# Optimization experiments

Measured on AMD Instinct MI355X. Metric: run time of the kernel, lower is better.

Reference implementation:

```python
import jax, jax.numpy as jnp
import numpy as np

IOU_THR = 0.5
SCORE_THR = 0.5
MAX_OUT = 300  # max_output_boxes_per_batch


def setup_inputs() -> dict:
    key = jax.random.key(0)
    kb, ks = jax.random.split(key)
    B, N, C = 8, 1024, 32
    u = jax.random.uniform(kb, (B, N, 4), dtype=jnp.float32)
    ctr = u[..., :2] * 100.0          # box centers in [0,100)
    sz = u[..., 2:] * 20.0 + 1.0      # box sizes in [1,21)
    # y1x1y2x2 format (as the torch module expects)
    boxes = jnp.concatenate([ctr - 0.5 * sz, ctr + 0.5 * sz], axis=-1)
    scores = jax.random.uniform(ks, (B, N, C), dtype=jnp.float32)
    return {"boxes": boxes, "scores": scores}


def _pairwise_iou(b):
    # b: [C, N, 4] in y1x1y2x2; IoU is invariant to the axis swap so no
    # conversion to x1y1x2y2 is needed.
    y1, x1, y2, x2 = b[..., 0], b[..., 1], b[..., 2], b[..., 3]
    area = (y2 - y1) * (x2 - x1)                          # [C, N]
    yy1 = jnp.maximum(y1[..., :, None], y1[..., None, :])
    xx1 = jnp.maximum(x1[..., :, None], x1[..., None, :])
    yy2 = jnp.minimum(y2[..., :, None], y2[..., None, :])
    xx2 = jnp.minimum(x2[..., :, None], x2[..., None, :])
    inter = jnp.clip(yy2 - yy1, 0.0) * jnp.clip(xx2 - xx1, 0.0)
    return inter / (area[..., :, None] + area[..., None, :] - inter)


def _nms_keep(iou, valid, thr):
    # Sequential greedy suppression, vectorized across classes.
    # iou: [C, N, N] (score-descending order), valid: [C, N] bool.
    N = iou.shape[-1]
    idx = jnp.arange(N)

    def body(i, keep):
        sup = (iou[:, i, :] > thr) & keep[:, i][:, None] & (idx[None, :] > i)
        return keep & ~sup

    return jax.lax.fori_loop(0, N, body, valid)


def _nms_single(boxes, scores):
    # boxes: [N, 4], scores: [N, C]  ->  ([M,4], [M], [M])
    N, C = scores.shape
    M = MAX_OUT
    sc = scores.T                                  # [C, N]
    valid = sc > SCORE_THR
    s = jnp.where(valid, sc, -jnp.inf)
    order = jnp.argsort(-s, axis=1, stable=True)   # per-class score desc
    sb = boxes[order]                              # [C, N, 4]
    ss = jnp.take_along_axis(s, order, axis=1)     # [C, N]
    sv = jnp.take_along_axis(valid, order, axis=1)
    keep = _nms_keep(_pairwise_iou(sb), sv, IOU_THR)   # [C, N]

    # flatten class-major (matches torch scores.transpose(1,0).flatten())
    fb = sb.reshape(C * N, 4)
    fs = ss.reshape(-1)
    fk = keep.reshape(-1)
    fcls = jnp.repeat(jnp.arange(C, dtype=jnp.int32), N)
    fbind = order.reshape(-1)                      # original box index

    # global score-descending order over kept detections, truncate to M
    g = jnp.where(fk, fs, -jnp.inf)
    gord = jnp.argsort(-g, stable=True)[:M]
    tb, ts, tc, ti, tv = fb[gord], fs[gord], fcls[gord], fbind[gord], fk[gord]

    # dedup by original box index: keep highest-score (first) occurrence;
    # torch's _get_unique_first_indices re-orders by ascending box index.
    p = jnp.arange(M, dtype=jnp.int32)
    first = jnp.full((N,), M, dtype=jnp.int32).at[ti].min(jnp.where(tv, p, M))
    present = first < M                            # [N]
    ordN = jnp.argsort(~present, stable=True)[:M]  # present box ids, ascending
    pos = first[ordN]
    m = present[ordN]
    posc = jnp.where(m, pos, 0)
    out_boxes = jnp.where(m[:, None], tb[posc], 0.0)
    out_scores = jnp.where(m, ts[posc], 0.0)
    out_classes = jnp.where(m, tc[posc], 0)
    return out_boxes, out_scores, out_classes


def reference(boxes, scores):
    ob, osc, ocl = jax.vmap(_nms_single)(boxes, scores)
    # matches torch return (output_boxes, output_scores, output_classes)
    return ob, osc, ocl
```

## Files before the change

### kernel.cpp

```cpp
#include <hip/hip_runtime.h>

#pragma clang fp contract(off)

#define NBOX   1024
#define NCLS   32
#define NBATCH 8
#define MAXOUT 300
#define SMAX   11
#define MAGIC  0x600DF00Du

#define IOU_SUP(ab, aa, bj, arj, act, acc) do {               \
    float yy1 = fmaxf((ab).x, (bj).x);                        \
    float xx1 = fmaxf((ab).y, (bj).y);                        \
    float yy2 = fminf((ab).z, (bj).z);                        \
    float xx2 = fminf((ab).w, (bj).w);                        \
    float ih = fmaxf(yy2 - yy1, 0.0f);                        \
    float iw = fmaxf(xx2 - xx1, 0.0f);                        \
    float inter = ih * iw;                                    \
    float denom = ((aa) + (arj)) - inter;                     \
    float lhs = (inter + inter) - denom;                      \
    float rhs = denom * 5.9604644775390625e-08f;              \
    if ((act) && (lhs > rhs)) (acc) |= bit;                   \
  } while (0)

__device__ __forceinline__ unsigned long long shflx64(unsigned long long v, int m) {
  unsigned lo = (unsigned)__shfl_xor((int)(unsigned)v, m, 64);
  unsigned hi = (unsigned)__shfl_xor((int)(unsigned)(v >> 32), m, 64);
  return ((unsigned long long)hi << 32) | lo;
}

__device__ __forceinline__ unsigned long long cexch(
    unsigned long long mine, int jj, int kk, int t) {
  unsigned long long other = shflx64(mine, jj);
  bool iLow = ((t & jj) == 0);
  bool desc = ((t & kk) == 0);
  bool wantMax = (iLow == desc);
  bool otherBigger = (other > mine);
  return (wantMax == otherBigger) ? other : mine;
}

__global__ __launch_bounds__(1024) void nms_fused(
    const float* __restrict__ boxes, const float* __restrict__ scores,
    unsigned long long* __restrict__ recs, unsigned int* __restrict__ flags,
    float* __restrict__ out) {
#pragma clang fp contract(off)
  const int bc = blockIdx.x;
  const int b = bc & (NBATCH - 1);
  const int c = bc >> 3;
  const int t = threadIdx.x;
  const int lane = t & 63, wav = t >> 6;

  __shared__ __align__(16) unsigned char shraw[63488];
  unsigned long long* key  = (unsigned long long*)shraw;
  float4* sbox             = (float4*)(shraw + 8192);
  float* sarea             = (float*)(shraw + 24576);
  unsigned long long* mask = (unsigned long long*)(shraw + 28672);
  __shared__ unsigned long long kb[16];
  __shared__ int shV;

  const float* sp = scores + (size_t)b * NBOX * NCLS + c;
  float s = sp[(size_t)t * NCLS];
  bool valid = (s > 0.5f);
  unsigned long long mine = valid
      ? ((((unsigned long long)__float_as_uint(s)) << 32) | (unsigned)(NBOX - 1 - t))
      : (unsigned long long)(unsigned)(NBOX - 1 - t);
  if (t == 0) shV = 0;
  if (t < 16) kb[t] = 0ull;
  __syncthreads();
  unsigned long long vb = __ballot(valid);
  if (lane == 0) atomicAdd(&shV, (int)__popcll(vb));

  for (int kk = 2; kk <= 64; kk <<= 1)
    for (int jj = kk >> 1; jj > 0; jj >>= 1)
      mine = cexch(mine, jj, kk, t);
  key[t] = mine;
  __syncthreads();
  for (int kk = 128; kk <= 1024; kk <<= 1) {
    for (int jj = kk >> 1; jj >= 64; jj >>= 1) {
      if (t < 512) {
        int i = ((t & ~(jj - 1)) << 1) | (t & (jj - 1));
        int ixj = i | jj;
        unsigned long long a = key[i], bb = key[ixj];
        if (((i & kk) == 0) ? (a < bb) : (a > bb)) { key[i] = bb; key[ixj] = a; }
      }
      __syncthreads();
    }
    mine = key[t];
    for (int jj = 32; jj > 0; jj >>= 1) mine = cexch(mine, jj, kk, t);
    key[t] = mine;
    __syncthreads();
  }

  int n0 = NBOX - 1 - (int)(mine & (NBOX - 1));
  const float4* gb = (const float4*)boxes + (size_t)b * NBOX;
  float4 bx4 = gb[n0];
  sbox[t] = bx4;
  sarea[t] = (bx4.z - bx4.x) * (bx4.w - bx4.y);
  __syncthreads();
  const int V = shV;
  const int S = (V + 63) >> 6;
  const bool aj = (t < V);

  unsigned long long mext[15];
  unsigned long long mself = 0ull;
#pragma unroll
  for (int w = 0; w < 15; ++w) mext[w] = 0ull;

  if (S <= SMAX) {
    int NC = 0;
    for (int I2 = 0; I2 < S; ++I2) NC += (S - I2 + 2) / 3;
    for (int k = wav; k < NC; k += 16) {
      int I = 0, rem = k;
      for (;;) { int cI = (S - I + 2) / 3; if (rem < cI) break; rem -= cI; ++I; }
      const int J0 = I + 3 * rem;
      const bool h1 = (J0 + 1 < S), h2 = (J0 + 2 < S);
      const int j0 = (J0 << 6) + lane;
      const int j1 = h1 ? j0 + 64 : j0;
      const int j2 = h2 ? j0 + 128 : j0;
      const float4 b0 = sbox[j0]; const float ar0 = sarea[j0];
      const float4 b1 = sbox[j1]; const float ar1 = sarea[j1];
      const float4 b2 = sbox[j2]; const float ar2 = sarea[j2];
      const bool act0 = (j0 < V);
      const bool act1 = h1 && (j0 + 64 < V);
      const bool act2 = h2 && (j0 + 128 < V);
      const float4* bi = &sbox[I << 6];
      const float* ai = &sarea[I << 6];
      unsigned long long a0 = 0, a1 = 0, a2 = 0;
      unsigned long long bit = 1ull;
#pragma unroll 8
      for (int q = 0; q < 64; ++q) {
        float4 ab = bi[q];
        float aa = ai[q];
        IOU_SUP(ab, aa, b0, ar0, act0, a0);
        IOU_SUP(ab, aa, b1, ar1, act1, a1);
        IOU_SUP(ab, aa, b2, ar2, act2, a2);
        bit <<= 1;
      }
      if (rem == 0) a0 &= (1ull << lane) - 1ull;
      const int vrem = V - (I << 6);
      if (vrem < 64) {
        unsigned long long tm = (1ull << vrem) - 1ull;
        a0 &= tm; a1 &= tm; a2 &= tm;
      }
      mask[(((J0 * (J0 + 1) / 2) << 6) + lane * (J0 + 1)) + I] = a0;
      if (h1) mask[((((J0 + 1) * (J0 + 2) / 2) << 6) + lane * (J0 + 2)) + I] = a1;
      if (h2) mask[((((J0 + 2) * (J0 + 3) / 2) << 6) + lane * (J0 + 3)) + I] = a2;
    }
    __syncthreads();
    if (t < (S << 6)) {
      const int J = wav;
      const int rbs = ((J * (J + 1) / 2) << 6) + lane * (J + 1);
#pragma unroll
      for (int I = 0; I < 15; ++I)
        if (I < J) mext[I] = mask[rbs + I];
      mself = mask[rbs + J];
    }
  } else {
    const int J = wav;
    const float4 bj = sbox[t];
    const float arj = sarea[t];
#pragma unroll
    for (int I = 0; I < 16; ++I) {
      if (I <= J && (I << 6) < V) {
        unsigned long long acc = 0, bit = 1ull;
        for (int q = 0; q < 64; ++q) {
          int i = (I << 6) + q;
          float4 ab = sbox[i];
          float aa = sarea[i];
          bool act = aj && (i < t) && (i < V);
          IOU_SUP(ab, aa, bj, arj, act, acc);
          bit <<= 1;
        }
        if (I == J) mself = acc;
        else mext[I] = acc;
      }
    }
  }
  __syncthreads();

  for (int w = 0; w < S; ++w) {
    if (wav == w) {
      bool supExt = false;
#pragma unroll
      for (int i = 0; i < 15; ++i)
        if (i < w) supExt = supExt || ((mext[i] & kb[i]) != 0ull);
      bool alive = aj && !supExt;
      unsigned long long cur = __ballot(alive);
      for (;;) {
        unsigned long long nb = __ballot(alive && ((mself & cur) == 0ull));
        if (nb == cur) break;
        cur = nb;
      }
      if (lane == 0) kb[w] = cur;
    }
    __syncthreads();
  }

  unsigned long long kbr[16];
#pragma unroll
  for (int w = 0; w < 16; ++w) kbr[w] = kb[w];
  int tot = 0;
#pragma unroll
  for (int w = 0; w < 16; ++w) tot += (int)__popcll(kbr[w]);
  const size_t rbase = ((size_t)b * NCLS + c) * MAXOUT;
  unsigned long long kw = kbr[0];
#pragma unroll
  for (int w = 1; w < 16; ++w) if (w == wav) kw = kbr[w];
  if (aj && ((kw >> lane) & 1ull)) {
    int rank = 0;
#pragma unroll
    for (int w = 0; w < 16; ++w)
      if (w < wav) rank += (int)__popcll(kbr[w]);
    rank += (int)__popcll(kw & ((1ull << lane) - 1ull));
    if (rank < MAXOUT) {
      unsigned sbits = (unsigned)(mine >> 32);
      int n = NBOX - 1 - (int)(mine & (NBOX - 1));
      int flat = c * NBOX + t;
      recs[rbase + rank] = (((unsigned long long)sbits) << 32)
          | ((unsigned)(NCLS * NBOX - 1 - flat) << 10) | (unsigned)n;
    }
  }
  if (t < MAXOUT && t >= ((tot < MAXOUT) ? tot : MAXOUT)) recs[rbase + t] = 0ull;

  __syncthreads();
  if (t == 0)
    __hip_atomic_store(&flags[bc], MAGIC, __ATOMIC_RELEASE,
                       __HIP_MEMORY_SCOPE_AGENT);
  if (c != 0) return;

  if (t < NCLS)
    while (__hip_atomic_load(&flags[(t << 3) + b], __ATOMIC_ACQUIRE,
                             __HIP_MEMORY_SCOPE_AGENT) != MAGIC)
      __builtin_amdgcn_s_sleep(8);
  __syncthreads();

  int* histw                 = (int*)shraw;
  int* hist                  = (int*)(shraw + 16384);
  int* suf                   = (int*)(shraw + 17408);
  unsigned long long* maxKey = (unsigned long long*)(shraw + 18448);
  unsigned long long* blist  = (unsigned long long*)(shraw + 26640);
  __shared__ int bcnt;
  __shared__ unsigned long long shT;
  __shared__ int shBstar;
  __shared__ int wcnt[16], woff[16];
  __shared__ int shPresTot;

  const int CAND = NCLS * MAXOUT;
  unsigned long long* rbp = recs + (size_t)b * NCLS * MAXOUT;
  unsigned long long cand[10];
#pragma unroll
  for (int q = 0; q < 10; ++q) {
    int j = t + (q << 10);
    cand[q] = (j < CAND)
        ? __hip_atomic_load(&rbp[j], __ATOMIC_RELAXED, __HIP_MEMORY_SCOPE_AGENT)
        : 0ull;
  }
  maxKey[t] = 0;
#pragma unroll
  for (int q = 0; q < 4; ++q) histw[t + (q << 10)] = 0;
  if (t == 0) { bcnt = 0; shT = 0; shBstar = -1; }
  __syncthreads();

#pragma unroll
  for (int q = 0; q < 10; ++q) {
    unsigned long long v = cand[q];
    if (v != 0ull) {
      int bk = (int)(((unsigned)(v >> 32) - 0x3F000000u) >> 15);
      atomicAdd(&histw[(wav << 8) + bk], 1);
    }
  }
  __syncthreads();
  if (t < 256) {
    int ssum = 0;
#pragma unroll
    for (int w = 0; w < 16; ++w) ssum += histw[(w << 8) + t];
    hist[t] = ssum;
  }
  __syncthreads();

  if (wav == 0) {
    int h[4];
#pragma unroll
    for (int g = 0; g < 4; ++g) h[g] = hist[g * 64 + lane];
#pragma unroll
    for (int g = 0; g < 4; ++g) {
      int v = h[g];
#pragma unroll
      for (int off = 1; off < 64; off <<= 1) {
        int u = __shfl_down(v, off);
        if (lane + off < 64) v += u;
      }
      h[g] = v;
    }
    int sum1 = __shfl(h[1], 0);
    int sum2 = __shfl(h[2], 0);
    int sum3 = __shfl(h[3], 0);
    suf[0 * 64 + lane] = h[0] + sum1 + sum2 + sum3;
    suf[1 * 64 + lane] = h[1] + sum2 + sum3;
    suf[2 * 64 + lane] = h[2] + sum3;
    suf[3 * 64 + lane] = h[3];
    if (lane == 0) suf[256] = 0;
  }
  __syncthreads();

  if (t < 256) {
    if (suf[t] >= MAXOUT && suf[t + 1] < MAXOUT) shBstar = t;
  }
  __syncthreads();
  const int Bstar = shBstar;

  if (Bstar >= 0) {
#pragma unroll
    for (int q = 0; q < 10; ++q) {
      unsigned long long v = cand[q];
      if (v != 0ull) {
        int bk = (int)(((unsigned)(v >> 32) - 0x3F000000u) >> 15);
        if (bk == Bstar) { int idx = atomicAdd(&bcnt, 1); blist[idx] = v; }
      }
    }
    __syncthreads();
    int M = bcnt;
    int need = MAXOUT - suf[Bstar + 1];
    if (t < M) {
      unsigned long long mk = blist[t];
      int r = 0;
      for (int i = 0; i < M; ++i) r += (blist[i] > mk) ? 1 : 0;
      if (r == need - 1) shT = mk;
    }
    __syncthreads();
  }
  const unsigned long long T = shT;

#pragma unroll
  for (int q = 0; q < 10; ++q) {
    unsigned long long v = cand[q];
    if (v != 0ull && v >= T) {
      int n = (int)(v & (NBOX - 1));
      atomicMax(&maxKey[n], v);
    }
  }
  __syncthreads();

  bool pres = (maxKey[t] != 0ull);
  unsigned long long wm = __ballot(pres);
  if (lane == 0) wcnt[wav] = (int)__popcll(wm);
  __syncthreads();
  if (t < 16) {
    int v = wcnt[t];
    int inc = v;
#pragma unroll
    for (int off = 1; off < 16; off <<= 1) {
      int u = __shfl_up(inc, off);
      if (lane >= off) inc += u;
    }
    woff[t] = inc - v;
    if (t == 15) shPresTot = inc;
  }
  __syncthreads();
  const int total = shPresTot;

  float* ob = out + (size_t)b * MAXOUT * 4;
  float* os = out + (size_t)NBATCH * MAXOUT * 4 + (size_t)b * MAXOUT;
  float* oc = out + (size_t)NBATCH * MAXOUT * 5 + (size_t)b * MAXOUT;

  if (pres) {
    int slot = woff[wav] + (int)__popcll(wm & ((1ull << lane) - 1ull));
    unsigned long long v = maxKey[t];
    float score = __uint_as_float((unsigned)(v >> 32));
    int flat = NCLS * NBOX - 1 - (int)((v >> 10) & (unsigned)(NCLS * NBOX - 1));
    int cls = flat >> 10;
    float4 bx = ((const float4*)boxes)[(size_t)b * NBOX + t];
    ob[slot * 4 + 0] = bx.x;
    ob[slot * 4 + 1] = bx.y;
    ob[slot * 4 + 2] = bx.z;
    ob[slot * 4 + 3] = bx.w;
    os[slot] = score;
    oc[slot] = (float)cls;
  }
  if (t >= total && t < MAXOUT) {
    ob[t * 4 + 0] = 0.0f; ob[t * 4 + 1] = 0.0f;
    ob[t * 4 + 2] = 0.0f; ob[t * 4 + 3] = 0.0f;
    os[t] = 0.0f;
    oc[t] = 0.0f;
  }
}

extern "C" void kernel_launch(void* const* d_in, const int* in_sizes, int n_in,
                              void* d_out, int out_size, void* d_ws, size_t ws_size,
                              hipStream_t stream) {
  const float* boxes  = (const float*)d_in[0];
  const float* scores = (const float*)d_in[1];
  float* out = (float*)d_out;

  unsigned long long* recs = (unsigned long long*)d_ws;
  unsigned int* flags = (unsigned int*)((char*)d_ws +
      (size_t)NBATCH * NCLS * MAXOUT * sizeof(unsigned long long));

  nms_fused<<<NBATCH * NCLS, 1024, 0, stream>>>(boxes, scores, recs, flags, out);
}
```

Measured before the change: 103.3 us.

## Replace block-wide bitonic sort with bucket sort and per-wave register bitonic

Valid scores (all in [0.5,1)) are bucketed into 16 buckets by the top mantissa bits. Ballots and a wave-level prefix scan scatter each key into a compact staging area. Each wave then sorts at most 64 keys of one bucket with a register-only shuffle bitonic network, which drops the many shared-memory passes and __syncthreads of the full 1024-element bitonic sort. If any bucket holds more than 64 keys, the code falls back to the original sort. Entries beyond V are left unsorted, which is fine because they are never used.

```diff
diff --git a/kernel.cpp b/kernel.cpp
--- a/kernel.cpp
+++ b/kernel.cpp
@@ -55,8 +55,11 @@
   float4* sbox             = (float4*)(shraw + 8192);
   float* sarea             = (float*)(shraw + 24576);
   unsigned long long* mask = (unsigned long long*)(shraw + 28672);
+  int* cnt                 = (int*)(shraw + 12288);
+  int* pre                 = (int*)(shraw + 13312);
+  unsigned* bstage32       = (unsigned*)(shraw + 16384);
   __shared__ unsigned long long kb[16];
-  __shared__ int shV;
+  __shared__ int shV, shOVF;
 
   const float* sp = scores + (size_t)b * NBOX * NCLS + c;
   float s = sp[(size_t)t * NCLS];
@@ -64,40 +67,103 @@
   unsigned long long mine = valid
       ? ((((unsigned long long)__float_as_uint(s)) << 32) | (unsigned)(NBOX - 1 - t))
       : (unsigned long long)(unsigned)(NBOX - 1 - t);
-  if (t == 0) shV = 0;
+  unsigned m23 = __float_as_uint(s) - 0x3F000000u;
+  int sbk = 15 - (int)(m23 >> 19);
+  unsigned key32 = ((m23 & 0x7FFFFu) << 10) | (unsigned)(NBOX - 1 - t);
+
+  if (t == 0) { shV = 0; shOVF = 0; }
   if (t < 16) kb[t] = 0ull;
   __syncthreads();
   unsigned long long vb = __ballot(valid);
   if (lane == 0) atomicAdd(&shV, (int)__popcll(vb));
 
-  for (int kk = 2; kk <= 64; kk <<= 1)
-    for (int jj = kk >> 1; jj > 0; jj >>= 1)
-      mine = cexch(mine, jj, kk, t);
-  key[t] = mine;
-  __syncthreads();
-  for (int kk = 128; kk <= 1024; kk <<= 1) {
-    for (int jj = kk >> 1; jj >= 64; jj >>= 1) {
-      if (t < 512) {
-        int i = ((t & ~(jj - 1)) << 1) | (t & (jj - 1));
-        int ixj = i | jj;
-        unsigned long long a = key[i], bb = key[ixj];
-        if (((i & kk) == 0) ? (a < bb) : (a > bb)) { key[i] = bb; key[ixj] = a; }
-      }
+  unsigned long long sel = 0ull;
+#pragma unroll
+  for (int bq = 0; bq < 16; ++bq) {
+    unsigned long long mm = __ballot(valid && (sbk == bq));
+    if (lane == bq) cnt[bq * 16 + wav] = (int)__popcll(mm);
+    if (sbk == bq) sel = mm;
+  }
+  __syncthreads();
+
+  if (wav == 0) {
+    int orig[4], inc[4];
+#pragma unroll
+    for (int g = 0; g < 4; ++g) { orig[g] = cnt[g * 64 + lane]; inc[g] = orig[g]; }
+#pragma unroll
+    for (int g = 0; g < 4; ++g)
+#pragma unroll
+      for (int off = 1; off < 64; off <<= 1) {
+        int u = __shfl_up(inc[g], off);
+        if (lane >= off) inc[g] += u;
+      }
+    int s0 = __builtin_amdgcn_readlane(inc[0], 63);
+    int s1 = __builtin_amdgcn_readlane(inc[1], 63);
+    int s2 = __builtin_amdgcn_readlane(inc[2], 63);
+    pre[0 * 64 + lane] = inc[0] - orig[0];
+    pre[1 * 64 + lane] = inc[1] - orig[1] + s0;
+    pre[2 * 64 + lane] = inc[2] - orig[2] + s0 + s1;
+    pre[3 * 64 + lane] = inc[3] - orig[3] + s0 + s1 + s2;
+  }
+  __syncthreads();
+  const int V = shV;
+  if (t < 16) {
+    int tb = ((t < 15) ? pre[(t + 1) * 16] : V) - pre[t * 16];
+    if (tb > 64) shOVF = 1;
+  }
+  __syncthreads();
+
+  if (!shOVF) {
+    if (valid) {
+      int rank = (int)__popcll(sel & ((1ull << lane) - 1ull));
+      bstage32[pre[sbk * 16 + wav] + rank] = key32;
+    }
+    __syncthreads();
+    const int start = pre[wav * 16];
+    const int cntb = ((wav < 15) ? pre[(wav + 1) * 16] : V) - start;
+    unsigned kreg = (lane < cntb) ? bstage32[start + lane] : 0u;
+    for (int kk2 = 2; kk2 <= 64; kk2 <<= 1)
+      for (int jj = kk2 >> 1; jj > 0; jj >>= 1) {
+        unsigned other = (unsigned)__shfl_xor((int)kreg, jj, 64);
+        bool wantMax = (((lane & jj) == 0) == ((lane & kk2) == 0));
+        kreg = (wantMax == (other > kreg)) ? other : kreg;
+      }
+    if (lane < cntb) {
+      unsigned sbits = 0x3F000000u + (((unsigned)(15 - wav)) << 19) + (kreg >> 10);
+      key[start + lane] = (((unsigned long long)sbits) << 32)
+          | (unsigned long long)(kreg & 1023u);
+    }
+    __syncthreads();
+  } else {
+    for (int kk = 2; kk <= 64; kk <<= 1)
+      for (int jj = kk >> 1; jj > 0; jj >>= 1)
+        mine = cexch(mine, jj, kk, t);
+    key[t] = mine;
+    __syncthreads();
+    for (int kk = 128; kk <= 1024; kk <<= 1) {
+      for (int jj = kk >> 1; jj >= 64; jj >>= 1) {
+        if (t < 512) {
+          int i = ((t & ~(jj - 1)) << 1) | (t & (jj - 1));
+          int ixj = i | jj;
+          unsigned long long a = key[i], bb = key[ixj];
+          if (((i & kk) == 0) ? (a < bb) : (a > bb)) { key[i] = bb; key[ixj] = a; }
+        }
+        __syncthreads();
+      }
+      mine = key[t];
+      for (int jj = 32; jj > 0; jj >>= 1) mine = cexch(mine, jj, kk, t);
+      key[t] = mine;
       __syncthreads();
     }
-    mine = key[t];
-    for (int jj = 32; jj > 0; jj >>= 1) mine = cexch(mine, jj, kk, t);
-    key[t] = mine;
-    __syncthreads();
-  }
-
-  int n0 = NBOX - 1 - (int)(mine & (NBOX - 1));
+  }
+
+  unsigned long long mykey = key[t];
+  int n0 = NBOX - 1 - (int)(mykey & (NBOX - 1));
   const float4* gb = (const float4*)boxes + (size_t)b * NBOX;
   float4 bx4 = gb[n0];
   sbox[t] = bx4;
   sarea[t] = (bx4.z - bx4.x) * (bx4.w - bx4.y);
   __syncthreads();
-  const int V = shV;
   const int S = (V + 63) >> 6;
   const bool aj = (t < V);
 
@@ -213,8 +279,8 @@
       if (w < wav) rank += (int)__popcll(kbr[w]);
     rank += (int)__popcll(kw & ((1ull << lane) - 1ull));
     if (rank < MAXOUT) {
-      unsigned sbits = (unsigned)(mine >> 32);
-      int n = NBOX - 1 - (int)(mine & (NBOX - 1));
+      unsigned sbits = (unsigned)(mykey >> 32);
+      int n = NBOX - 1 - (int)(mykey & (NBOX - 1));
       int flat = c * NBOX + t;
       recs[rbase + rank] = (((unsigned long long)sbits) << 32)
           | ((unsigned)(NCLS * NBOX - 1 - flat) << 10) | (unsigned)n;
```

Result: faster. 99.69 us (-3.5%).
